# Kernel optimization log

Measured on AMD Instinct MI355X. Metric: run time of the kernel, lower is better.

The kernel has to match this reference:

```python
import jax, jax.numpy as jnp
import numpy as np

B, L, D = 8, 2048, 1024


def _hippo(d, seed=0):
    # Author's 'hippo_matrix': Q @ diag(arctan(linspace(0, pi, d))) @ Q.T with Q orthogonal.
    rng = np.random.default_rng(seed)
    Q, _ = np.linalg.qr(rng.standard_normal((d, d)))
    Dm = np.diag(np.arctan(np.linspace(0.0, np.pi, d)))
    return (Q @ Dm @ Q.T).astype(np.float32)


def setup_inputs() -> dict:
    key = jax.random.key(0)
    k1, k2, k3, k4 = jax.random.split(key, 4)
    x = jax.random.normal(k1, (B, L, D), jnp.float32)
    A_w = jnp.asarray(_hippo(D))                                   # [D, D], spectral norm <= arctan(pi)
    C_w = jax.random.normal(k2, (D, D), jnp.float32) * (D ** -0.5)  # readout C
    # rc maps cat(x_t, y_{t-1}, y_container) (3D) -> D; small init keeps the
    # linear recurrence spectral radius < 1 so the 2048-step scan stays finite.
    rc_w = jax.random.normal(k3, (D, 3 * D), jnp.float32) * (0.2 / np.sqrt(3 * D))
    rc_b = jax.random.normal(k4, (D,), jnp.float32) * 0.02
    return {"x": x, "A_w": A_w, "C_w": C_w, "rc_w": rc_w, "rc_b": rc_b}


def reference(x, A_w, C_w, rc_w, rc_b):
    # y[0] = x[0]; y[t] = C @ A @ (rc_w @ cat(x[t], y[t-1], y[t-1]) + rc_b)
    # (prev output enters twice: once via the outer forward_step cat, once via
    #  the LinearRecurrentContainer's internal memory y).
    d = x.shape[-1]
    Wx = rc_w[:, :d]                          # acts on x_t
    Wy = rc_w[:, d:2 * d] + rc_w[:, 2 * d:]   # both copies of y_{t-1}
    M = C_w @ A_w                             # fused C∘A readout, [D, D]
    P = M @ Wx                                # input map
    Q = M @ Wy                                # recurrence map
    c = M @ rc_b                              # fused bias
    u = jnp.einsum('bld,ed->ble', x[:, 1:], P) + c  # driving terms for t >= 1, [B, L-1, D]
    y0 = x[:, 0]                              # parallel_scan copies the first input verbatim

    def step(y_prev, u_t):
        y = u_t + y_prev @ Q.T                # [B, D]
        return y, y

    _, ys = jax.lax.scan(step, y0, jnp.swapaxes(u, 0, 1))  # [L-1, B, D]
    return jnp.concatenate([y0[:, None, :], jnp.swapaxes(ys, 0, 1)], axis=1)  # [B, L, D]
```

## Files before the change

kernel.cpp:

```cpp
#include <hip/hip_runtime.h>

typedef unsigned short u16;
typedef unsigned int   u32;
typedef __attribute__((ext_vector_type(8))) short short8;
typedef __attribute__((ext_vector_type(4))) short short4v;
typedef __attribute__((ext_vector_type(4))) float f32x4;

struct SqJobs {
  const u16* a[4];
  const u16* b[4];
  u16* c[4];
  u16* ct[4];
};

__device__ __forceinline__ float bf2f(u16 v) {
  u32 x = ((u32)v) << 16;
  return __builtin_bit_cast(float, x);
}
__device__ __forceinline__ u16 f2bf(float f) {
  u32 x = __builtin_bit_cast(u32, f);
  x += 0x7FFFu + ((x >> 16) & 1u);
  return (u16)(x >> 16);
}
__device__ __forceinline__ void gload_lds16(const u16* g, u16* l) {
  __builtin_amdgcn_global_load_lds(
      (const __attribute__((address_space(1))) u32*)g,
      (__attribute__((address_space(3))) u32*)l, 16, 0, 0);
}

template <int BM, int BN, int ADT, int BDT, int EPI, int AMAP, int OMAP,
          int COUT, int TRW, int SQF>
__global__ __launch_bounds__(256) void gemm_nt(
    const void* __restrict__ Av, int lda, const void* __restrict__ Bv, int ldb,
    void* __restrict__ Cv, int ldc, int Mrows, int K,
    const float* __restrict__ zrowF, const u16* __restrict__ zrowB,
    const float* __restrict__ bias, const float* __restrict__ addf,
    float* __restrict__ Yout, u16* __restrict__ aux16, int jp1, int shoff,
    SqJobs jb) {
  constexpr int WM = BM / 2, WN = BN / 2;
  constexpr int MT = WM / 16, NTT = WN / 16;
  constexpr int AIn = ADT ? BM * 8 : BM * 4;
  constexpr int BIn = BDT ? BN * 8 : BN * 4;
  static_assert(AIn >= 256 && BIn >= 256, "tile too small for 256 threads");
  constexpr int AI = AIn / 256, BI = BIn / 256;
  __shared__ u16 lA[BM * 32];
  __shared__ u16 lB[BN * 32];
  const int tid = threadIdx.x;
  const int lane = tid & 63, wid = tid >> 6;
  const int wm = wid & 1, wn = wid >> 1;
  const bool role = (SQF == 1) && ((int)blockIdx.x >= 32);
  const int pi = role ? (((int)blockIdx.x - 32) >> 4) : 0;
  const int bxe = role ? (((int)blockIdx.x - 32) & 15) : (int)blockIdx.x;
  const int m0 = bxe * BM, n0 = blockIdx.y * BN;
  const int effM = role ? 1024 : Mrows;
  const int q = lane >> 4, lm = lane & 15;
  const int cq = (q ^ (lm & 3)) * 8;

  const u16* corrB = nullptr;
  if constexpr (EPI == 7)
    corrB = (blockIdx.z == 0)
                ? (const u16*)Bv
                : jb.a[0] + (long)((int)blockIdx.z - 1) * 1048576;

  f32x4 acc[MT][NTT];
#pragma unroll
  for (int mi = 0; mi < MT; ++mi)
#pragma unroll
    for (int ni = 0; ni < NTT; ++ni) acc[mi][ni] = (f32x4){0.f, 0.f, 0.f, 0.f};

  const u16* aB[AI];
  const float* aF[AI];
#pragma unroll
  for (int i = 0; i < AI; ++i) {
    int g = tid + i * 256;
    int r = ADT ? (g >> 3) : (g >> 2);
    int c = ADT ? (g & 7) : (g & 3);
    int row = m0 + r;
    bool valid = (row < effM);
    if (AMAP == 1 && !role) {
      int p = row % 257;
      if (p < shoff) valid = false;
      row -= shoff;
    }
    if constexpr (ADT == 1) {
      int cs = ((((c >> 1) ^ (r & 3)) << 1) | (c & 1)) * 4;
      aF[i] = (valid ? (const float*)Av + (long)row * lda : zrowF) + cs;
    } else {
      int cs = (c ^ (r & 3)) * 8;
      const u16* base;
      if (role)
        base = jb.a[pi] + (long)row * 1024;
      else
        base = valid ? (const u16*)Av + (long)row * lda : zrowB;
      aB[i] = base + cs;
    }
  }
  const u16* bB[BI];
  const float* bF[BI];
#pragma unroll
  for (int i = 0; i < BI; ++i) {
    int g = tid + i * 256;
    int r = BDT ? (g >> 3) : (g >> 2);
    int c = BDT ? (g & 7) : (g & 3);
    if constexpr (BDT == 1) {
      int cs = ((((c >> 1) ^ (r & 3)) << 1) | (c & 1)) * 4;
      bF[i] = (const float*)Bv + (long)(n0 + r) * ldb + cs;
    } else {
      int cs = (c ^ (r & 3)) * 8;
      const u16* base;
      if (role) {
        base = jb.b[pi] + (long)(n0 + r) * 1024;
      } else {
        if constexpr (EPI == 7)
          base = corrB + (long)(n0 + r) * ldb;
        else
          base = (const u16*)Bv + (long)(n0 + r) * ldb;
      }
      bB[i] = base + cs;
    }
  }

  for (int k0 = 0; k0 < K; k0 += 32) {
    f32x4 fa[AI], fb[BI];
    if constexpr (ADT == 1) {
#pragma unroll
      for (int i = 0; i < AI; ++i) fa[i] = *(const f32x4*)(aF[i] + k0);
    }
    if constexpr (BDT == 1) {
#pragma unroll
      for (int i = 0; i < BI; ++i) fb[i] = *(const f32x4*)(bF[i] + k0);
    }
    __syncthreads();
    if constexpr (ADT == 0) {
#pragma unroll
      for (int i = 0; i < AI; ++i)
        gload_lds16(aB[i] + k0, &lA[(tid + i * 256) * 8]);
    } else {
#pragma unroll
      for (int i = 0; i < AI; ++i) {
        short4v s = {(short)f2bf(fa[i][0]), (short)f2bf(fa[i][1]),
                     (short)f2bf(fa[i][2]), (short)f2bf(fa[i][3])};
        *(short4v*)&lA[(tid + i * 256) * 4] = s;
      }
    }
    if constexpr (BDT == 0) {
#pragma unroll
      for (int i = 0; i < BI; ++i)
        gload_lds16(bB[i] + k0, &lB[(tid + i * 256) * 8]);
    } else {
#pragma unroll
      for (int i = 0; i < BI; ++i) {
        short4v s = {(short)f2bf(fb[i][0]), (short)f2bf(fb[i][1]),
                     (short)f2bf(fb[i][2]), (short)f2bf(fb[i][3])};
        *(short4v*)&lB[(tid + i * 256) * 4] = s;
      }
    }
    __syncthreads();
    short8 af[MT], bf[NTT];
#pragma unroll
    for (int mi = 0; mi < MT; ++mi)
      af[mi] = *(const short8*)&lA[(wm * WM + mi * 16 + lm) * 32 + cq];
#pragma unroll
    for (int ni = 0; ni < NTT; ++ni)
      bf[ni] = *(const short8*)&lB[(wn * WN + ni * 16 + lm) * 32 + cq];
#pragma unroll
    for (int mi = 0; mi < MT; ++mi)
#pragma unroll
      for (int ni = 0; ni < NTT; ++ni)
        acc[mi][ni] = __builtin_amdgcn_mfma_f32_16x16x32_bf16(
            af[mi], bf[ni], acc[mi][ni], 0, 0, 0);
  }

#pragma unroll
  for (int mi = 0; mi < MT; ++mi) {
    int rbase = m0 + wm * WM + mi * 16 + q * 4;
#pragma unroll
    for (int ni = 0; ni < NTT; ++ni) {
      int ocol = n0 + wn * WN + ni * 16 + lm;
#pragma unroll
      for (int r = 0; r < 4; ++r) {
        int orow = rbase + r;
        float v = acc[mi][ni][r];
        if (role) {
          if (orow < 1024) {
            u16 ov = f2bf(v);
            jb.c[pi][(long)orow * 1024 + ocol] = ov;
            if (jb.ct[pi]) jb.ct[pi][(long)ocol * 1024 + orow] = ov;
          }
          continue;
        }
        if (orow >= Mrows) continue;
        if constexpr (EPI == 7) {
          long urow = 8L * orow + ((int)blockIdx.z + 1);
          float vv = v + addf[urow * 1024 + ocol];
          Yout[urow * 1024 + ocol] = vv;
          continue;
        }
        if constexpr (EPI == 5) {
          v += bias[ocol];
          bool isT0 = (orow & 2047) == 0;
          if (isT0) v = addf[(long)orow * 1024 + ocol];
          ((float*)Cv)[(long)orow * ldc + ocol] = v;
          if (isT0) Yout[((long)(orow >> 11) * 257) * 1024 + ocol] = v;
          if ((orow & 7) == 1)
            aux16[((long)(orow >> 3)) * 1024 + ocol] = f2bf(v);
          continue;
        }
        if constexpr (EPI == 6) {
          v += addf[(long)orow * 1024 + ocol];
          ((float*)Cv)[(long)orow * ldc + ocol] = v;
          int b = orow / 257;
          int pp_ = orow - b * 257;
          if (pp_ < 256)
            aux16[((long)(b * 256 + pp_)) * 1024 + ocol] = f2bf(v);
          if (pp_ >= 1 && pp_ < 256)
            Yout[((long)b * 2048 + 8L * pp_) * 1024 + ocol] = v;
          continue;
        }
        long urow = 0;
        bool uok = true;
        if constexpr (EPI == 2 || EPI == 3) {
          urow = 8L * orow + jp1;
          uok = ((urow & 2047) != 0);
          if (uok) v += addf[urow * 1024 + ocol];
        }
        if constexpr (EPI == 4) v += addf[(long)orow * 1024 + ocol];
        long wrow = orow;
        if constexpr (OMAP == 1)
          wrow = (long)(orow >> 8) * 257 + (orow & 255) + 1;
        if constexpr (COUT == 1)
          ((float*)Cv)[wrow * (long)ldc + ocol] = v;
        else
          ((u16*)Cv)[wrow * (long)ldc + ocol] = f2bf(v);
        if constexpr (TRW == 1) aux16[(long)ocol * ldc + orow] = f2bf(v);
        if constexpr (EPI == 3) {
          if (uok) Yout[urow * 1024 + ocol] = v;
        }
      }
    }
  }
}

__global__ void zero_misc(float* zF, u16* zB) {
  for (int i = threadIdx.x; i < 2048; i += 256) {
    zF[i] = 0.f;
    zB[i] = 0;
  }
}
__global__ void xconv(const float* __restrict__ x, u16* __restrict__ xb) {
  long i = (long)blockIdx.x * 256 + threadIdx.x;
  f32x4 v = ((const f32x4*)x)[i];
  short4v s = {(short)f2bf(v[0]), (short)f2bf(v[1]), (short)f2bf(v[2]),
               (short)f2bf(v[3])};
  ((short4v*)xb)[i] = s;
}
__global__ void prep_wt(const float* __restrict__ rc_w, u16* __restrict__ WxT,
                        u16* __restrict__ WyT) {
  __shared__ u16 tx[64][65];
  __shared__ u16 ty[64][65];
  int kb = blockIdx.x * 64, db = blockIdx.y * 64;
  for (int i = threadIdx.x; i < 64 * 64; i += 256) {
    int r = i >> 6, c = i & 63;
    long base = (long)(kb + r) * 3072 + db + c;
    tx[r][c] = f2bf(rc_w[base]);
    ty[r][c] = f2bf(rc_w[base + 1024] + rc_w[base + 2048]);
  }
  __syncthreads();
  for (int i = threadIdx.x; i < 64 * 64; i += 256) {
    int r = i >> 6, c = i & 63;
    WxT[(long)(db + r) * 1024 + kb + c] = tx[c][r];
    WyT[(long)(db + r) * 1024 + kb + c] = ty[c][r];
  }
}
__global__ void matvec_c(const u16* __restrict__ M_,
                         const float* __restrict__ rb,
                         float* __restrict__ cvec) {
  int row = blockIdx.x;
  int lane = threadIdx.x;
  float s = 0.f;
  for (int k = lane; k < 1024; k += 64)
    s += bf2f(M_[(long)row * 1024 + k]) * rb[k];
  for (int o = 32; o > 0; o >>= 1) s += __shfl_down(s, o, 64);
  if (lane == 0) cvec[row] = s;
}

extern "C" void kernel_launch(void* const* d_in, const int* in_sizes, int n_in,
                              void* d_out, int out_size, void* d_ws,
                              size_t ws_size, hipStream_t stream) {
  const float* x = (const float*)d_in[0];
  const float* A_w = (const float*)d_in[1];
  const float* C_w = (const float*)d_in[2];
  const float* rc_w = (const float*)d_in[3];
  const float* rc_b = (const float*)d_in[4];
  float* Y = (float*)d_out;

  char* ws = (char*)d_ws;
  const long MB = 1 << 20;
  u16* Z0 = (u16*)(ws);
  u16* Z1 = (u16*)(ws + 4 * MB);
  float* Bnd0 = (float*)(ws + 8 * MB);
  float* Bnd1 = (float*)(ws + 8 * MB + 8912896);
  char* p = ws + 25 * MB;
  u16* Mbuf = (u16*)p;
  u16* WxT = (u16*)(p + 2 * MB);
  u16* WyT = (u16*)(p + 4 * MB);
  u16* Pbuf = (u16*)(p + 6 * MB);
  u16* Qbuf = (u16*)(p + 8 * MB);
  u16* QbufT = (u16*)(p + 10 * MB);
  float* cvec = (float*)(p + 12 * MB);
  float* zF = (float*)(p + 12 * MB + 4096);
  u16* zB = (u16*)(p + 12 * MB + 12288);
  u16* xbf = (u16*)(p + 12 * MB + 16384);
  const size_t need_fast = (size_t)(25 * MB + 12 * MB + 16384) + 33554432;
  const bool fast = ws_size >= need_fast;

  SqJobs J0{};
  dim3 blk(256);
  zero_misc<<<dim3(1), blk, 0, stream>>>(zF, zB);
  if (fast) xconv<<<dim3(16384), blk, 0, stream>>>(x, xbf);
  prep_wt<<<dim3(16, 16), blk, 0, stream>>>(rc_w, WxT, WyT);

  gemm_nt<64, 64, 1, 1, 0, 0, 0, 0, 0, 0><<<dim3(16, 16), blk, 0, stream>>>(
      C_w, 1024, A_w, 1024, Mbuf, 1024, 1024, 1024, zF, zB, nullptr, nullptr,
      nullptr, nullptr, 0, 0, J0);
  gemm_nt<64, 64, 0, 0, 0, 0, 0, 0, 0, 0><<<dim3(16, 16), blk, 0, stream>>>(
      Mbuf, 1024, WxT, 1024, Pbuf, 1024, 1024, 1024, zF, zB, nullptr, nullptr,
      nullptr, nullptr, 0, 0, J0);
  gemm_nt<64, 64, 0, 0, 0, 0, 0, 0, 1, 0><<<dim3(16, 16), blk, 0, stream>>>(
      Mbuf, 1024, WyT, 1024, Qbuf, 1024, 1024, 1024, zF, zB, nullptr, nullptr,
      nullptr, QbufT, 0, 0, J0);
  matvec_c<<<dim3(1024), dim3(64), 0, stream>>>(Mbuf, rc_b, cvec);

  if (fast)
    gemm_nt<128, 128, 0, 0, 5, 0, 0, 1, 0, 0>
        <<<dim3(128, 8), blk, 0, stream>>>(xbf, 1024, Pbuf, 1024, Y, 1024,
                                           16384, 1024, zF, zB, cvec, x, Bnd0,
                                           Z0, 0, 0, J0);
  else
    gemm_nt<128, 128, 1, 0, 5, 0, 0, 1, 0, 0>
        <<<dim3(128, 8), blk, 0, stream>>>(x, 1024, Pbuf, 1024, Y, 1024, 16384,
                                           1024, zF, zB, cvec, x, Bnd0, Z0, 0,
                                           0, J0);

  if (fast) {
    const long M1 = 1048576;
    u16* PW = xbf;
    u16* Q2 = PW + 0 * M1;
    u16* Q3 = PW + 1 * M1;
    u16* Q4 = PW + 2 * M1;
    u16* Q5 = PW + 3 * M1;
    u16* Q6 = PW + 4 * M1;
    u16* Q7 = PW + 5 * M1;
    u16* Tb2 = xbf + 6 * M1;
    u16* Tt2 = xbf + 7 * M1;
    u16* Tb3 = xbf + 8 * M1;
    u16* Tt3 = xbf + 9 * M1;
    u16* Tb4 = xbf + 10 * M1;
    u16* Tt4 = xbf + 11 * M1;
    u16* Tb5 = xbf + 12 * M1;
    u16* Tt5 = xbf + 13 * M1;
    u16* Tb6 = xbf + 14 * M1;
    u16* Tt6 = xbf + 15 * M1;
    u16* Tt0 = Mbuf;
    u16* Tt1 = WxT;
    u16* Pw3T = WyT;

    SqJobs sj[7] = {};
    int nsq[7] = {1, 2, 4, 1, 1, 1, 1};
    sj[0].a[0] = Qbuf;  sj[0].b[0] = QbufT; sj[0].c[0] = Q2;  sj[0].ct[0] = Tt0;
    sj[1].a[0] = Q2;    sj[1].b[0] = Tt0;   sj[1].c[0] = Q4;  sj[1].ct[0] = Tt1;
    sj[1].a[1] = Q2;    sj[1].b[1] = QbufT; sj[1].c[1] = Q3;  sj[1].ct[1] = Pw3T;
    sj[2].a[0] = Q4;    sj[2].b[0] = Tt1;   sj[2].c[0] = Tb2; sj[2].ct[0] = Tt2;
    sj[2].a[1] = Q4;    sj[2].b[1] = QbufT; sj[2].c[1] = Q5;
    sj[2].a[2] = Q4;    sj[2].b[2] = Tt0;   sj[2].c[2] = Q6;
    sj[2].a[3] = Q4;    sj[2].b[3] = Pw3T;  sj[2].c[3] = Q7;
    sj[3].a[0] = Tb2;   sj[3].b[0] = Tt2;   sj[3].c[0] = Tb3; sj[3].ct[0] = Tt3;
    sj[4].a[0] = Tb3;   sj[4].b[0] = Tt3;   sj[4].c[0] = Tb4; sj[4].ct[0] = Tt4;
    sj[5].a[0] = Tb4;   sj[5].b[0] = Tt4;   sj[5].c[0] = Tb5; sj[5].ct[0] = Tt5;
    sj[6].a[0] = Tb5;   sj[6].b[0] = Tt5;   sj[6].c[0] = Tb6; sj[6].ct[0] = Tt6;

    for (int j = 1; j <= 6; ++j) {
      const u16* zin = (j & 1) ? Z0 : Z1;
      u16* zout = (j & 1) ? Z1 : Z0;
      gemm_nt<64, 64, 0, 0, 3, 0, 0, 0, 0, 1>
          <<<dim3(32 + 16 * nsq[j - 1], 16), blk, 0, stream>>>(
              zin, 1024, Qbuf, 1024, zout, 1024, 2048, 1024, zF, zB, nullptr,
              Y, Y, nullptr, j + 1, 0, sj[j - 1]);
    }
    gemm_nt<64, 64, 0, 0, 2, 0, 1, 1, 0, 1><<<dim3(48, 16), blk, 0, stream>>>(
        Z0, 1024, Qbuf, 1024, Bnd0, 1024, 2048, 1024, zF, zB, nullptr, Y,
        nullptr, nullptr, 8, 0, sj[6]);

    u16* TbP2[5] = {Tb2, Tb3, Tb4, Tb5, Tb6};
    float* bc = Bnd0;
    float* bn = Bnd1;
    for (int s = 0; s < 5; ++s) {
      if (s < 4)
        gemm_nt<64, 64, 1, 0, 4, 1, 0, 1, 0, 0>
            <<<dim3(33, 16), blk, 0, stream>>>(bc, 1024, TbP2[s], 1024, bn,
                                               1024, 2056, 1024, zF, zB,
                                               nullptr, bc, nullptr, nullptr,
                                               0, 1 << s, J0);
      else
        gemm_nt<64, 64, 1, 0, 6, 1, 0, 1, 0, 0>
            <<<dim3(33, 16), blk, 0, stream>>>(bc, 1024, TbP2[s], 1024, bn,
                                               1024, 2056, 1024, zF, zB,
                                               nullptr, bc, Y, Z0, 0, 1 << s,
                                               J0);
      float* t = bc;
      bc = bn;
      bn = t;
    }

    SqJobs cj{};
    cj.a[0] = PW;
    gemm_nt<64, 64, 0, 0, 7, 0, 0, 0, 0, 0>
        <<<dim3(32, 16, 7), blk, 0, stream>>>(Z0, 1024, Qbuf, 1024, Z1, 1024,
                                              2048, 1024, zF, zB, nullptr, Y,
                                              Y, nullptr, 0, 0, cj);
  } else {
    u16* Tb[7];
    u16* Tt[7];
    for (int i = 0; i < 7; ++i) {
      Tb[i] = (i & 1) ? Mbuf : WxT;
      Tt[i] = (i & 1) ? Pbuf : WyT;
    }
    for (int j = 1; j <= 6; ++j) {
      const u16* zin = (j & 1) ? Z0 : Z1;
      u16* zout = (j & 1) ? Z1 : Z0;
      gemm_nt<64, 64, 0, 0, 2, 0, 0, 0, 0, 0>
          <<<dim3(32, 16), blk, 0, stream>>>(zin, 1024, Qbuf, 1024, zout, 1024,
                                             2048, 1024, zF, zB, nullptr, Y,
                                             nullptr, nullptr, j + 1, 0, J0);
    }
    gemm_nt<64, 64, 0, 0, 2, 0, 1, 1, 0, 0><<<dim3(32, 16), blk, 0, stream>>>(
        Z0, 1024, Qbuf, 1024, Bnd0, 1024, 2048, 1024, zF, zB, nullptr, Y,
        nullptr, nullptr, 8, 0, J0);
    for (int i = 0; i < 3; ++i) {
      const u16* si = (i == 0) ? Qbuf : Tb[i - 1];
      const u16* st = (i == 0) ? QbufT : Tt[i - 1];
      gemm_nt<64, 64, 0, 0, 0, 0, 0, 0, 1, 0>
          <<<dim3(16, 16), blk, 0, stream>>>(si, 1024, st, 1024, Tb[i], 1024,
                                             1024, 1024, zF, zB, nullptr,
                                             nullptr, nullptr, Tt[i], 0, 0,
                                             J0);
    }
    float* bc = Bnd0;
    float* bn = Bnd1;
    for (int s = 0; s < 5; ++s) {
      if (s < 4)
        gemm_nt<64, 64, 1, 0, 4, 1, 0, 1, 0, 0>
            <<<dim3(33, 16), blk, 0, stream>>>(bc, 1024, Tb[s + 2], 1024, bn,
                                               1024, 2056, 1024, zF, zB,
                                               nullptr, bc, nullptr, nullptr,
                                               0, 1 << s, J0);
      else
        gemm_nt<64, 64, 1, 0, 6, 1, 0, 1, 0, 0>
            <<<dim3(33, 16), blk, 0, stream>>>(bc, 1024, Tb[s + 2], 1024, bn,
                                               1024, 2056, 1024, zF, zB,
                                               nullptr, bc, Y, Z0, 0, 1 << s,
                                               J0);
      if (s < 4) {
        int i = s + 3;
        gemm_nt<64, 64, 0, 0, 0, 0, 0, 0, 1, 0>
            <<<dim3(16, 16), blk, 0, stream>>>(Tb[i - 1], 1024, Tt[i - 1],
                                               1024, Tb[i], 1024, 1024, 1024,
                                               zF, zB, nullptr, nullptr,
                                               nullptr, Tt[i], 0, 0, J0);
      }
      float* t = bc;
      bc = bn;
      bn = t;
    }
    for (int j = 0; j <= 7; ++j) {
      const u16* zin = (j & 1) ? Z1 : Z0;
      u16* zout = (j & 1) ? Z0 : Z1;
      gemm_nt<64, 64, 0, 0, 3, 0, 0, 0, 0, 0>
          <<<dim3(32, 16), blk, 0, stream>>>(zin, 1024, Qbuf, 1024, zout, 1024,
                                             2048, 1024, zF, zB, nullptr, Y, Y,
                                             nullptr, j + 1, 0, J0);
    }
  }
}
```

Measured before the change: 660.3 us.

## Double-buffer LDS tiles in GEMM to overlap global loads with MFMA

Doubles the shared-memory A/B tiles and prefetches the next K-slice into the alternate buffer while MFMAs run on the current one, removing one barrier per iteration. For fp32 inputs the conversion and LDS store are moved after the MFMAs so load latency is hidden. This uses twice the LDS, which may reduce occupancy, and the single barrier must be enough to keep reads and writes of the two buffers from conflicting.

```diff
diff --git a/kernel.cpp b/kernel.cpp
--- a/kernel.cpp
+++ b/kernel.cpp
@@ -43,8 +43,9 @@
   constexpr int BIn = BDT ? BN * 8 : BN * 4;
   static_assert(AIn >= 256 && BIn >= 256, "tile too small for 256 threads");
   constexpr int AI = AIn / 256, BI = BIn / 256;
-  __shared__ u16 lA[BM * 32];
-  __shared__ u16 lB[BN * 32];
+  constexpr int LA = BM * 32, LB = BN * 32;
+  __shared__ u16 lA[2 * LA];
+  __shared__ u16 lB[2 * LB];
   const int tid = threadIdx.x;
   const int lane = tid & 63, wid = tid >> 6;
   const int wm = wid & 1, wn = wid >> 1;
@@ -120,55 +121,95 @@
     }
   }
 
+  if constexpr (ADT == 1) {
+    f32x4 f0[AI];
+#pragma unroll
+    for (int i = 0; i < AI; ++i) f0[i] = *(const f32x4*)(aF[i]);
+#pragma unroll
+    for (int i = 0; i < AI; ++i) {
+      short4v s = {(short)f2bf(f0[i][0]), (short)f2bf(f0[i][1]),
+                   (short)f2bf(f0[i][2]), (short)f2bf(f0[i][3])};
+      *(short4v*)&lA[(tid + i * 256) * 4] = s;
+    }
+  } else {
+#pragma unroll
+    for (int i = 0; i < AI; ++i) gload_lds16(aB[i], &lA[(tid + i * 256) * 8]);
+  }
+  if constexpr (BDT == 1) {
+    f32x4 f0[BI];
+#pragma unroll
+    for (int i = 0; i < BI; ++i) f0[i] = *(const f32x4*)(bF[i]);
+#pragma unroll
+    for (int i = 0; i < BI; ++i) {
+      short4v s = {(short)f2bf(f0[i][0]), (short)f2bf(f0[i][1]),
+                   (short)f2bf(f0[i][2]), (short)f2bf(f0[i][3])};
+      *(short4v*)&lB[(tid + i * 256) * 4] = s;
+    }
+  } else {
+#pragma unroll
+    for (int i = 0; i < BI; ++i) gload_lds16(bB[i], &lB[(tid + i * 256) * 8]);
+  }
+  __syncthreads();
+
+  int cur = 0;
   for (int k0 = 0; k0 < K; k0 += 32) {
+    const int kn = k0 + 32;
+    const bool more = kn < K;
+    const int nxA = (cur ^ 1) * LA, nxB = (cur ^ 1) * LB;
     f32x4 fa[AI], fb[BI];
-    if constexpr (ADT == 1) {
-#pragma unroll
-      for (int i = 0; i < AI; ++i) fa[i] = *(const f32x4*)(aF[i] + k0);
-    }
-    if constexpr (BDT == 1) {
-#pragma unroll
-      for (int i = 0; i < BI; ++i) fb[i] = *(const f32x4*)(bF[i] + k0);
-    }
-    __syncthreads();
-    if constexpr (ADT == 0) {
-#pragma unroll
-      for (int i = 0; i < AI; ++i)
-        gload_lds16(aB[i] + k0, &lA[(tid + i * 256) * 8]);
-    } else {
-#pragma unroll
-      for (int i = 0; i < AI; ++i) {
-        short4v s = {(short)f2bf(fa[i][0]), (short)f2bf(fa[i][1]),
-                     (short)f2bf(fa[i][2]), (short)f2bf(fa[i][3])};
-        *(short4v*)&lA[(tid + i * 256) * 4] = s;
-      }
-    }
-    if constexpr (BDT == 0) {
-#pragma unroll
-      for (int i = 0; i < BI; ++i)
-        gload_lds16(bB[i] + k0, &lB[(tid + i * 256) * 8]);
-    } else {
-#pragma unroll
-      for (int i = 0; i < BI; ++i) {
-        short4v s = {(short)f2bf(fb[i][0]), (short)f2bf(fb[i][1]),
-                     (short)f2bf(fb[i][2]), (short)f2bf(fb[i][3])};
-        *(short4v*)&lB[(tid + i * 256) * 4] = s;
-      }
-    }
-    __syncthreads();
+    if (more) {
+      if constexpr (ADT == 1) {
+#pragma unroll
+        for (int i = 0; i < AI; ++i) fa[i] = *(const f32x4*)(aF[i] + kn);
+      } else {
+#pragma unroll
+        for (int i = 0; i < AI; ++i)
+          gload_lds16(aB[i] + kn, &lA[nxA + (tid + i * 256) * 8]);
+      }
+      if constexpr (BDT == 1) {
+#pragma unroll
+        for (int i = 0; i < BI; ++i) fb[i] = *(const f32x4*)(bF[i] + kn);
+      } else {
+#pragma unroll
+        for (int i = 0; i < BI; ++i)
+          gload_lds16(bB[i] + kn, &lB[nxB + (tid + i * 256) * 8]);
+      }
+    }
     short8 af[MT], bf[NTT];
 #pragma unroll
     for (int mi = 0; mi < MT; ++mi)
-      af[mi] = *(const short8*)&lA[(wm * WM + mi * 16 + lm) * 32 + cq];
+      af[mi] =
+          *(const short8*)&lA[cur * LA + (wm * WM + mi * 16 + lm) * 32 + cq];
 #pragma unroll
     for (int ni = 0; ni < NTT; ++ni)
-      bf[ni] = *(const short8*)&lB[(wn * WN + ni * 16 + lm) * 32 + cq];
+      bf[ni] =
+          *(const short8*)&lB[cur * LB + (wn * WN + ni * 16 + lm) * 32 + cq];
 #pragma unroll
     for (int mi = 0; mi < MT; ++mi)
 #pragma unroll
       for (int ni = 0; ni < NTT; ++ni)
         acc[mi][ni] = __builtin_amdgcn_mfma_f32_16x16x32_bf16(
             af[mi], bf[ni], acc[mi][ni], 0, 0, 0);
+    if (more) {
+      if constexpr (ADT == 1) {
+#pragma unroll
+        for (int i = 0; i < AI; ++i) {
+          short4v s = {(short)f2bf(fa[i][0]), (short)f2bf(fa[i][1]),
+                       (short)f2bf(fa[i][2]), (short)f2bf(fa[i][3])};
+          *(short4v*)&lA[nxA + (tid + i * 256) * 4] = s;
+        }
+      }
+      if constexpr (BDT == 1) {
+#pragma unroll
+        for (int i = 0; i < BI; ++i) {
+          short4v s = {(short)f2bf(fb[i][0]), (short)f2bf(fb[i][1]),
+                       (short)f2bf(fb[i][2]), (short)f2bf(fb[i][3])};
+          *(short4v*)&lB[nxB + (tid + i * 256) * 4] = s;
+        }
+      }
+    }
+    __syncthreads();
+    cur ^= 1;
   }
 
 #pragma unroll
```

Measured after the change: 649.9 us. About the same (-1.6%).
